# Kernel optimization log

Measured on AMD Instinct MI355X. Metric: run time of the kernel, lower is better.

## Reference

```python
import jax, jax.numpy as jnp
import numpy as np

VOCAB, EMB, HID, B, T = 32000, 1024, 1024, 16, 256

def setup_inputs() -> dict:
    key = jax.random.key(0)
    ks = jax.random.split(key, 9)
    s = 0.02
    return {
        "x": jax.random.randint(ks[0], (B, T), 0, VOCAB, dtype=jnp.int64),
        "hidden": jnp.zeros((2, B, HID), dtype=jnp.float32),
        "emb_W": jax.random.normal(ks[1], (VOCAB, EMB), dtype=jnp.float32) * s,  # tied with output proj
        "Wx0": jax.random.normal(ks[2], (EMB, HID), dtype=jnp.float32) * s,
        "Wh0": jax.random.normal(ks[3], (HID, HID), dtype=jnp.float32) * s,
        "b0": jnp.zeros((HID,), dtype=jnp.float32),
        "Wx1": jax.random.normal(ks[4], (HID, HID), dtype=jnp.float32) * s,
        "Wh1": jax.random.normal(ks[5], (HID, HID), dtype=jnp.float32) * s,
        "b1": jnp.zeros((HID,), dtype=jnp.float32),
        "out_b": jnp.zeros((VOCAB,), dtype=jnp.float32),
    }

def reference(x, hidden, emb_W, Wx0, Wh0, b0, Wx1, Wh1, b1, out_b):
    emb = emb_W[x]                      # (B, T, EMB)
    emb_t = jnp.swapaxes(emb, 0, 1)     # (T, B, EMB) time-major for scan

    def step(h, e):
        h0, h1 = h
        h0n = jnp.tanh(e @ Wx0 + h0 @ Wh0 + b0)      # layer 0 cell
        h1n = jnp.tanh(h0n @ Wx1 + h1 @ Wh1 + b1)    # layer 1 cell
        logits = h1n @ emb_W.T + out_b               # tied output projection
        return (h0n, h1n), logits

    (h0f, h1f), logits_t = jax.lax.scan(step, (hidden[0], hidden[1]), emb_t)
    logits = jnp.swapaxes(logits_t, 0, 1)            # (B, T, VOCAB)
    return logits, jnp.stack([h0f, h1f])             # final hidden (2, B, HID)
```

## Files before the change

kernel.cpp:

```cpp
#include <hip/hip_runtime.h>
#include <stdint.h>

#define VOCAB 32000
#define EMB   1024
#define HID   1024
#define BATCH 16
#define SEQ   256
#define MROWS (SEQ*BATCH)

typedef unsigned short u16;
typedef uint32_t u32;
typedef __bf16 bf16x8 __attribute__((ext_vector_type(8)));
typedef float  f32x4  __attribute__((ext_vector_type(4)));
typedef u32    u32x4  __attribute__((ext_vector_type(4)));

static __device__ __forceinline__ u16 f2bf(float f) {
  union { float f; uint32_t u; } v; v.f = f;
  return (u16)((v.u + 0x7FFFu + ((v.u >> 16) & 1u)) >> 16);
}

static __device__ __forceinline__ f32x4 MFMA(bf16x8 a, bf16x8 b, f32x4 c) {
  return __builtin_amdgcn_mfma_f32_16x16x32_bf16(a, b, c, 0, 0, 0);
}


static __device__ __forceinline__ void loadt8(const void* p, u32x4* r) {
  asm volatile(
    "global_load_dwordx4 %0, %8, off sc0 sc1\n\t"
    "global_load_dwordx4 %1, %8, off offset:16 sc0 sc1\n\t"
    "global_load_dwordx4 %2, %8, off offset:128 sc0 sc1\n\t"
    "global_load_dwordx4 %3, %8, off offset:144 sc0 sc1\n\t"
    "global_load_dwordx4 %4, %8, off offset:256 sc0 sc1\n\t"
    "global_load_dwordx4 %5, %8, off offset:272 sc0 sc1\n\t"
    "global_load_dwordx4 %6, %8, off offset:384 sc0 sc1\n\t"
    "global_load_dwordx4 %7, %8, off offset:400 sc0 sc1\n\t"
    "s_waitcnt vmcnt(0)"
    : "=&v"(r[0]), "=&v"(r[1]), "=&v"(r[2]), "=&v"(r[3]),
      "=&v"(r[4]), "=&v"(r[5]), "=&v"(r[6]), "=&v"(r[7])
    : "v"(p) : "memory");
}

static __device__ __forceinline__ void loadt16(const void* p, u32x4* r) {
  asm volatile(
    "global_load_dwordx4 %0, %16, off sc0 sc1\n\t"
    "global_load_dwordx4 %1, %16, off offset:16 sc0 sc1\n\t"
    "global_load_dwordx4 %2, %16, off offset:128 sc0 sc1\n\t"
    "global_load_dwordx4 %3, %16, off offset:144 sc0 sc1\n\t"
    "global_load_dwordx4 %4, %16, off offset:256 sc0 sc1\n\t"
    "global_load_dwordx4 %5, %16, off offset:272 sc0 sc1\n\t"
    "global_load_dwordx4 %6, %16, off offset:384 sc0 sc1\n\t"
    "global_load_dwordx4 %7, %16, off offset:400 sc0 sc1\n\t"
    "global_load_dwordx4 %8, %16, off offset:512 sc0 sc1\n\t"
    "global_load_dwordx4 %9, %16, off offset:528 sc0 sc1\n\t"
    "global_load_dwordx4 %10, %16, off offset:640 sc0 sc1\n\t"
    "global_load_dwordx4 %11, %16, off offset:656 sc0 sc1\n\t"
    "global_load_dwordx4 %12, %16, off offset:768 sc0 sc1\n\t"
    "global_load_dwordx4 %13, %16, off offset:784 sc0 sc1\n\t"
    "global_load_dwordx4 %14, %16, off offset:896 sc0 sc1\n\t"
    "global_load_dwordx4 %15, %16, off offset:912 sc0 sc1\n\t"
    "s_waitcnt vmcnt(0)"
    : "=&v"(r[0]), "=&v"(r[1]), "=&v"(r[2]), "=&v"(r[3]),
      "=&v"(r[4]), "=&v"(r[5]), "=&v"(r[6]), "=&v"(r[7]),
      "=&v"(r[8]), "=&v"(r[9]), "=&v"(r[10]), "=&v"(r[11]),
      "=&v"(r[12]), "=&v"(r[13]), "=&v"(r[14]), "=&v"(r[15])
    : "v"(p) : "memory");
}

static __device__ __forceinline__ void load22(const void* p0, const void* p1, u32x4* r) {
  asm volatile(
    "global_load_dwordx4 %0, %4, off sc0 sc1\n\t"
    "global_load_dwordx4 %1, %4, off offset:16 sc0 sc1\n\t"
    "global_load_dwordx4 %2, %5, off sc0 sc1\n\t"
    "global_load_dwordx4 %3, %5, off offset:16 sc0 sc1\n\t"
    "s_waitcnt vmcnt(0)"
    : "=&v"(r[0]), "=&v"(r[1]), "=&v"(r[2]), "=&v"(r[3])
    : "v"(p0), "v"(p1) : "memory");
}

static __device__ __forceinline__ void store_u32_coh(u32* p, u32 v) {
  asm volatile("global_store_dword %0, %1, off sc0 sc1"
               :: "v"(p), "v"(v) : "memory");
}
static __device__ __forceinline__ void store_u16_coh(u16* p, u16 v) {
  asm volatile("global_store_short %0, %1, off sc0 sc1"
               :: "v"(p), "v"((u32)v) : "memory");
}
static __device__ __forceinline__ void wait_vm0() {
  asm volatile("s_waitcnt vmcnt(0)" ::: "memory");
}

static __device__ __forceinline__ int flags_ready(const void* p, u32 pat) {
  u32x4 a, b, c, d;
  asm volatile(
    "global_load_dwordx4 %0, %4, off sc0 sc1\n\t"
    "global_load_dwordx4 %1, %4, off offset:16 sc0 sc1\n\t"
    "global_load_dwordx4 %2, %4, off offset:32 sc0 sc1\n\t"
    "global_load_dwordx4 %3, %4, off offset:48 sc0 sc1\n\t"
    "s_waitcnt vmcnt(0)"
    : "=&v"(a), "=&v"(b), "=&v"(c), "=&v"(d)
    : "v"(p) : "memory");
  u32 m = (a[0]^pat)|(a[1]^pat)|(a[2]^pat)|(a[3]^pat)
        | (b[0]^pat)|(b[1]^pat)|(b[2]^pat)|(b[3]^pat)
        | (c[0]^pat)|(c[1]^pat)|(c[2]^pat)|(c[3]^pat)
        | (d[0]^pat)|(d[1]^pat)|(d[2]^pat)|(d[3]^pat);
  return m == 0u;
}

static __device__ __forceinline__ bf16x8 packfrag(u32x4 e, u32x4 o) {
  u32x4 p;
  p[0] = (e[1] << 16) | (e[0] & 0xFFFFu);
  p[1] = (e[3] << 16) | (e[2] & 0xFFFFu);
  p[2] = (o[1] << 16) | (o[0] & 0xFFFFu);
  p[3] = (o[3] << 16) | (o[2] & 0xFFFFu);
  union { u32x4 u; bf16x8 b; } c; c.u = p; return c.b;
}


__global__ void cvt_hidden(const float* __restrict__ hidden,
                           u16* __restrict__ h0i, u16* __restrict__ h1i,
                           unsigned* __restrict__ flags) {
  int i = blockIdx.x * 256 + threadIdx.x;
  if (i < 16384) flags[i] = 0u;
  if (i < BATCH * HID)            h0i[i] = f2bf(hidden[i]);
  else if (i < 2 * BATCH * HID)   h1i[i - BATCH * HID] = f2bf(hidden[i]);
}

__global__ void transpose_cvt(const float* __restrict__ in, u16* __restrict__ out) {
  __shared__ float tile[32][33];
  int bx = blockIdx.x * 32;
  int by = blockIdx.y * 32;
  int tx = threadIdx.x, ty = threadIdx.y;
  #pragma unroll
  for (int i = 0; i < 32; i += 8)
    tile[ty + i][tx] = in[(size_t)(by + ty + i) * HID + bx + tx];
  __syncthreads();
  #pragma unroll
  for (int i = 0; i < 32; i += 8)
    out[(size_t)(bx + ty + i) * HID + by + tx] = f2bf(tile[tx][ty + i]);
}

__global__ void cvt_emb(const float4* __restrict__ in, ushort4* __restrict__ out, int n4) {
  int stride = gridDim.x * blockDim.x;
  for (int i = blockIdx.x * blockDim.x + threadIdx.x; i < n4; i += stride) {
    float4 v = in[i];
    ushort4 o; o.x = f2bf(v.x); o.y = f2bf(v.y); o.z = f2bf(v.z); o.w = f2bf(v.w);
    out[i] = o;
  }
}

__global__ void gather_emb(const int* __restrict__ x, const float* __restrict__ embW,
                           u16* __restrict__ E) {
  int r = blockIdx.x;
  int b = r & 15, t = r >> 4;
  int idx = x[b * SEQ + t];
  const float4* src = (const float4*)(embW + (size_t)idx * EMB);
  ushort4* dst = (ushort4*)(E + (size_t)r * EMB);
  float4 v = src[threadIdx.x];
  ushort4 o; o.x = f2bf(v.x); o.y = f2bf(v.y); o.z = f2bf(v.z); o.w = f2bf(v.w);
  dst[threadIdx.x] = o;
}

__global__ __launch_bounds__(256) void gemm_bt(
    const u16* __restrict__ A, const u16* __restrict__ B,
    const float* __restrict__ bias, float* __restrict__ C,
    int M, int N, int K)
{
  __shared__ __align__(16) char lds[32768];
  char* As = lds;
  char* Bs = lds + 16384;
  const int tid  = threadIdx.x;
  const int lane = tid & 63;
  const int wave = tid >> 6;
  const int wr = wave >> 1, wc = wave & 1;
  const int bm = blockIdx.y * 128;
  const int bn = blockIdx.x * 128;
  const int srow = tid >> 3;
  const int swc  = (tid & 7) ^ (srow & 7);

  f32x4 acc[4][4];
  #pragma unroll
  for (int i = 0; i < 4; ++i)
    #pragma unroll
    for (int j = 0; j < 4; ++j) acc[i][j] = (f32x4){0.f, 0.f, 0.f, 0.f};

  const u16* Ab = A + (size_t)(bm + srow) * K + swc * 8;
  const u16* Bb = B + (size_t)(bn + srow) * K + swc * 8;
  const size_t rstep = (size_t)32 * K;

  for (int k0 = 0; k0 < K; k0 += 64) {
    #pragma unroll
    for (int i = 0; i < 4; ++i) {
      __builtin_amdgcn_global_load_lds(
          (const __attribute__((address_space(1))) void*)(Ab + i * rstep + k0),
          (__attribute__((address_space(3))) void*)(As + i * 4096 + wave * 1024),
          16, 0, 0);
      __builtin_amdgcn_global_load_lds(
          (const __attribute__((address_space(1))) void*)(Bb + i * rstep + k0),
          (__attribute__((address_space(3))) void*)(Bs + i * 4096 + wave * 1024),
          16, 0, 0);
    }
    __syncthreads();
    #pragma unroll
    for (int ks = 0; ks < 2; ++ks) {
      bf16x8 af[4], bq[4];
      #pragma unroll
      for (int mi = 0; mi < 4; ++mi) {
        int row = wr * 64 + mi * 16 + (lane & 15);
        int c = (ks * 4 + (lane >> 4)) ^ (row & 7);
        af[mi] = *(const bf16x8*)(As + row * 128 + c * 16);
      }
      #pragma unroll
      for (int ni = 0; ni < 4; ++ni) {
        int row = wc * 64 + ni * 16 + (lane & 15);
        int c = (ks * 4 + (lane >> 4)) ^ (row & 7);
        bq[ni] = *(const bf16x8*)(Bs + row * 128 + c * 16);
      }
      #pragma unroll
      for (int mi = 0; mi < 4; ++mi)
        #pragma unroll
        for (int ni = 0; ni < 4; ++ni)
          acc[mi][ni] = MFMA(af[mi], bq[ni], acc[mi][ni]);
    }
    __syncthreads();
  }

  #pragma unroll
  for (int mi = 0; mi < 4; ++mi) {
    #pragma unroll
    for (int ni = 0; ni < 4; ++ni) {
      const int col = bn + wc * 64 + ni * 16 + (lane & 15);
      const float bv = bias[col];
      #pragma unroll
      for (int j = 0; j < 4; ++j) {
        const int row = bm + wr * 64 + mi * 16 + ((lane >> 4) << 2) + j;
        C[(size_t)row * N + col] = acc[mi][ni][j] + bv;
      }
    }
  }
}

#define NB0L 32
#define RL_NREC 64
#define LOG_TN 250
#define COMB_OFF 131072
#define LDS_TOTAL (COMB_OFF + 16384)

__global__ __launch_bounds__(512) void rec_logits(
    const u16* __restrict__ Wh0T, const u16* __restrict__ Wx1T, const u16* __restrict__ Wh1T,
    const float* __restrict__ X0, const float* __restrict__ b1,
    const u16* __restrict__ h0init, const u16* __restrict__ h1init,
    u32* H0u, u32* H1u,
    const u16* __restrict__ embB, const float* __restrict__ outb,
    float* out, char* flags)
{
  __shared__ __align__(16) char lds[LDS_TOTAL];
  const int tid  = threadIdx.x;
  const int lane = tid & 63;
  const int w    = tid >> 6;
  const int l15  = lane & 15;
  const int lk   = lane >> 4;
  const int blk  = blockIdx.x;
  f32x4* cmb = (f32x4*)(lds + COMB_OFF);
  float* hidOut = out + (size_t)BATCH * SEQ * VOCAB;

  if (blk >= RL_NREC) {
    const int lb = blk - RL_NREC;
    const int tm = lb / LOG_TN;
    const int tn = lb - tm * LOG_TN;
    const int bm = tm * 128, bn = tn * 128;
    if (tid == 0) {
      const u32 pat = (u32)(tm + 1) * 0x10001u;
      while (!flags_ready(flags + (size_t)tm * 128, pat)) __builtin_amdgcn_s_sleep(8);
    }
    __syncthreads();

    char* As = lds;
    char* Bs = lds + 16384;
    const int wr = w >> 2, wc = w & 3;
    const int srow = tid >> 3;
    const int sch  = (tid & 7) ^ (srow & 7);
    const u16* Bb  = embB + (size_t)(bn + srow) * EMB + sch * 8;
    const u32* Ab0 = H1u + (size_t)(bm + srow) * HID + sch * 8;
    const u32* Ab1 = H1u + (size_t)(bm + 64 + srow) * HID + sch * 8;
    char* Ad0 = As + srow * 128 + (tid & 7) * 16;
    char* Ad1 = As + (64 + srow) * 128 + (tid & 7) * 16;

    f32x4 acc[4][2];
    #pragma unroll
    for (int mi = 0; mi < 4; ++mi)
      #pragma unroll
      for (int ni = 0; ni < 2; ++ni) acc[mi][ni] = (f32x4){0.f, 0.f, 0.f, 0.f};

    for (int k0 = 0; k0 < EMB; k0 += 64) {
      #pragma unroll
      for (int i = 0; i < 2; ++i)
        __builtin_amdgcn_global_load_lds(
            (const __attribute__((address_space(1))) void*)(Bb + (size_t)i * 64 * EMB + k0),
            (__attribute__((address_space(3))) void*)(Bs + i * 8192 + w * 1024 + lane * 16),
            16, 0, 0);
      u32x4 ra[4];
      load22(Ab0 + k0, Ab1 + k0, ra);
      union { u32x4 u; bf16x8 b; } c0, c1;
      c0.b = packfrag(ra[0], ra[1]);
      c1.b = packfrag(ra[2], ra[3]);
      *(u32x4*)Ad0 = c0.u;
      *(u32x4*)Ad1 = c1.u;
      __syncthreads();
      #pragma unroll
      for (int ks = 0; ks < 2; ++ks) {
        bf16x8 af[4], bq[2];
        #pragma unroll
        for (int mi = 0; mi < 4; ++mi) {
          int row = wr * 64 + mi * 16 + l15;
          int c = (ks * 4 + lk) ^ (row & 7);
          af[mi] = *(const bf16x8*)(As + row * 128 + c * 16);
        }
        #pragma unroll
        for (int ni = 0; ni < 2; ++ni) {
          int row = wc * 32 + ni * 16 + l15;
          int c = (ks * 4 + lk) ^ (row & 7);
          bq[ni] = *(const bf16x8*)(Bs + row * 128 + c * 16);
        }
        #pragma unroll
        for (int mi = 0; mi < 4; ++mi)
          #pragma unroll
          for (int ni = 0; ni < 2; ++ni)
            acc[mi][ni] = MFMA(af[mi], bq[ni], acc[mi][ni]);
      }
      __syncthreads();
    }
    #pragma unroll
    for (int ni = 0; ni < 2; ++ni) {
      const int col = bn + wc * 32 + ni * 16 + l15;
      const float bv = outb[col];
      #pragma unroll
      for (int mi = 0; mi < 4; ++mi) {
        #pragma unroll
        for (int j = 0; j < 4; ++j) {
          const int row = bm + wr * 64 + mi * 16 + lk * 4 + j;
          out[(size_t)(row & 15) * ((size_t)SEQ * VOCAB)
              + (size_t)(row >> 4) * VOCAB + col] = acc[mi][ni][j] + bv;
        }
      }
    }
    return;
  }

  const bool is0 = (blk < NB0L);
  if (is0) {
    const u16* src = Wh0T + (size_t)(blk * 32) * HID;
    for (int it = 0; it < 8; ++it) {
      int g = it * 512 + tid;
      int brow = g & 31, f = g >> 5;
      *(bf16x8*)(lds + f * 512 + brow * 16) =
          *(const bf16x8*)(src + (size_t)brow * HID + f * 8);
    }
  } else {
    const u16* s0 = Wx1T + (size_t)((blk - NB0L) * 32) * HID;
    const u16* s1 = Wh1T + (size_t)((blk - NB0L) * 32) * HID;
    for (int it = 0; it < 8; ++it) {
      int g = it * 512 + tid;
      int brow = g & 31, f = g >> 5;
      int o = f * 512 + brow * 16;
      *(bf16x8*)(lds + o)         = *(const bf16x8*)(s0 + (size_t)brow * HID + f * 8);
      *(bf16x8*)(lds + 65536 + o) = *(const bf16x8*)(s1 + (size_t)brow * HID + f * 8);
    }
  }
  __syncthreads();

  if (is0) {
    const int col = blk * 32 + w * 16 + l15;
    const char* H0b = (const char*)H0u + (size_t)l15 * 4096 + (size_t)w * 512 + lk * 32;
    for (int s = 0; s < SEQ; ++s) {
      float xv[4];
      if (w < 2) {
        #pragma unroll
        for (int j = 0; j < 4; ++j)
          xv[j] = X0[(size_t)(s * BATCH + lk * 4 + j) * HID + col];
      }
      bf16x8 a[4];
      if (s == 0) {
        const char* p = (const char*)h0init + l15 * 2048 + w * 256 + lk * 16;
        #pragma unroll
        for (int m = 0; m < 4; ++m) a[m] = *(const bf16x8*)(p + m * 64);
      } else {
        u32x4 r[8];
        const void* hb = H0b + (size_t)(s - 1) * 65536;
        const u32 tagw = (u32)s << 16;
        for (;;) {
          loadt8(hb, r);
          u32 acc = 0;
          #pragma unroll
          for (int i = 0; i < 8; ++i)
            #pragma unroll
            for (int j = 0; j < 4; ++j) acc |= r[i][j] ^ tagw;
          if (__all((acc & 0xFFFF0000u) == 0u)) break;
        }
        #pragma unroll
        for (int m = 0; m < 4; ++m) a[m] = packfrag(r[2 * m], r[2 * m + 1]);
      }
      f32x4 acc0 = {0,0,0,0}, acc1 = {0,0,0,0};
      #pragma unroll
      for (int m = 0; m < 4; ++m) {
        const int f = (w * 4 + m) * 4 + lk;
        acc0 = MFMA(a[m], *(const bf16x8*)(lds + f * 512 + l15 * 16),        acc0);
        acc1 = MFMA(a[m], *(const bf16x8*)(lds + f * 512 + (16 + l15) * 16), acc1);
      }
      cmb[(w * 2 + 0) * 64 + lane] = acc0;
      cmb[(w * 2 + 1) * 64 + lane] = acc1;
      __syncthreads();
      if (w < 2) {
        f32x4 r = (cmb[(0 * 2 + w) * 64 + lane] + cmb[(1 * 2 + w) * 64 + lane])
                + (cmb[(2 * 2 + w) * 64 + lane] + cmb[(3 * 2 + w) * 64 + lane])
                + (cmb[(4 * 2 + w) * 64 + lane] + cmb[(5 * 2 + w) * 64 + lane])
                + (cmb[(6 * 2 + w) * 64 + lane] + cmb[(7 * 2 + w) * 64 + lane]);
        #pragma unroll
        for (int j = 0; j < 4; ++j) {
          const int b = lk * 4 + j;
          float v = tanhf(r[j] + xv[j]);
          u32 word = ((u32)(s + 1) << 16) | (u32)f2bf(v);
          store_u32_coh(H0u + (size_t)(s * BATCH + b) * HID + col, word);
          if (s == SEQ - 1) hidOut[(size_t)b * HID + col] = v;
        }
      }
      __syncthreads();
    }
  } else {
    const int lblk = blk - NB0L;
    const int m2 = w >> 2;
    const int q  = w & 3;
    const int col = lblk * 32 + w * 16 + l15;
    const float bv = (w < 2) ? b1[col] : 0.f;
    const char* wb = lds + m2 * 65536;
    const size_t lbase = (size_t)l15 * 4096 + (size_t)q * 1024 + lk * 32;
    for (int t = 0; t < SEQ; ++t) {
      bf16x8 a[8];
      if (m2 == 1 && t == 0) {
        const char* p = (const char*)h1init + l15 * 2048 + q * 512 + lk * 16;
        #pragma unroll
        for (int m = 0; m < 8; ++m) a[m] = *(const bf16x8*)(p + m * 64);
      } else {
        const void* hb = (m2 == 0)
            ? (const void*)((const char*)H0u + (size_t)t * 65536 + lbase)
            : (const void*)((const char*)H1u + (size_t)(t - 1) * 65536 + lbase);
        const u32 tagw = (u32)(m2 == 0 ? t + 1 : t) << 16;
        u32x4 r[16];
        for (;;) {
          loadt16(hb, r);
          u32 acc = 0;
          #pragma unroll
          for (int i = 0; i < 16; ++i)
            #pragma unroll
            for (int j = 0; j < 4; ++j) acc |= r[i][j] ^ tagw;
          if (__all((acc & 0xFFFF0000u) == 0u)) break;
        }
        #pragma unroll
        for (int m = 0; m < 8; ++m) a[m] = packfrag(r[2 * m], r[2 * m + 1]);
      }
      f32x4 acc0 = {0,0,0,0}, acc1 = {0,0,0,0};
      #pragma unroll
      for (int m = 0; m < 8; ++m) {
        const int f = (q * 8 + m) * 4 + lk;
        acc0 = MFMA(a[m], *(const bf16x8*)(wb + f * 512 + l15 * 16),        acc0);
        acc1 = MFMA(a[m], *(const bf16x8*)(wb + f * 512 + (16 + l15) * 16), acc1);
      }
      cmb[(w * 2 + 0) * 64 + lane] = acc0;
      cmb[(w * 2 + 1) * 64 + lane] = acc1;
      __syncthreads();
      if (w < 2) {
        f32x4 r = (cmb[(0 * 2 + w) * 64 + lane] + cmb[(1 * 2 + w) * 64 + lane])
                + (cmb[(2 * 2 + w) * 64 + lane] + cmb[(3 * 2 + w) * 64 + lane])
                + (cmb[(4 * 2 + w) * 64 + lane] + cmb[(5 * 2 + w) * 64 + lane])
                + (cmb[(6 * 2 + w) * 64 + lane] + cmb[(7 * 2 + w) * 64 + lane]);
        #pragma unroll
        for (int j = 0; j < 4; ++j) {
          const int b = lk * 4 + j;
          float v = tanhf(r[j] + bv);
          u32 word = ((u32)(t + 1) << 16) | (u32)f2bf(v);
          store_u32_coh(H1u + (size_t)(t * BATCH + b) * HID + col, word);
          if (t == SEQ - 1)
            hidOut[(size_t)(BATCH * HID) + (size_t)b * HID + col] = v;
        }
        if ((t & 7) == 7) wait_vm0();
      }
      __syncthreads();
      if (((t & 7) == 7) && tid == 0)
        store_u16_coh((u16*)(flags + (size_t)(t >> 3) * 128) + lblk, (u16)((t >> 3) + 1));
    }
  }
}

extern "C" void kernel_launch(void* const* d_in, const int* in_sizes, int n_in,
                              void* d_out, int out_size, void* d_ws, size_t ws_size,
                              hipStream_t stream) {
  const int*   x      = (const int*)  d_in[0];
  const float* hidden = (const float*)d_in[1];
  const float* embW   = (const float*)d_in[2];
  const float* Wx0    = (const float*)d_in[3];
  const float* Wh0    = (const float*)d_in[4];
  const float* b0     = (const float*)d_in[5];
  const float* Wx1    = (const float*)d_in[6];
  const float* Wh1    = (const float*)d_in[7];
  const float* b1     = (const float*)d_in[8];
  const float* outb   = (const float*)d_in[9];
  float* out = (float*)d_out;

  char* ws = (char*)d_ws;
  size_t off = 0;
  auto alloc = [&](size_t bytes) {
    char* p = ws + off; off += (bytes + 255) & ~(size_t)255; return p;
  };
  u16*   embB = (u16*)  alloc((size_t)VOCAB * EMB * 2);
  u16*   Wx0T = (u16*)  alloc((size_t)EMB * HID * 2);
  u16*   Wh0T = (u16*)  alloc((size_t)HID * HID * 2);
  u16*   Wx1T = (u16*)  alloc((size_t)HID * HID * 2);
  u16*   Wh1T = (u16*)  alloc((size_t)HID * HID * 2);
  u16*   E    = (u16*)  alloc((size_t)MROWS * EMB * 2);
  float* X0f  = (float*)alloc((size_t)MROWS * HID * 4);
  u32*   H0u  = (u32*)  alloc((size_t)MROWS * HID * 4);
  u32*   H1u  = (u32*)  alloc((size_t)MROWS * HID * 4);
  u16*   h0i  = (u16*)  alloc((size_t)BATCH * HID * 2);
  u16*   h1i  = (u16*)  alloc((size_t)BATCH * HID * 2);
  char*  flags = (char*)alloc(65536);
  if (off > ws_size) return;

  cvt_hidden<<<dim3(128), dim3(256), 0, stream>>>(hidden, h0i, h1i, (unsigned*)flags);

  dim3 tb(32, 8), tg(32, 32);
  transpose_cvt<<<tg, tb, 0, stream>>>(Wx0, Wx0T);
  transpose_cvt<<<tg, tb, 0, stream>>>(Wh0, Wh0T);
  transpose_cvt<<<tg, tb, 0, stream>>>(Wx1, Wx1T);
  transpose_cvt<<<tg, tb, 0, stream>>>(Wh1, Wh1T);

  cvt_emb<<<dim3(2048), dim3(256), 0, stream>>>(
      (const float4*)embW, (ushort4*)embB, (int)((size_t)VOCAB * EMB / 4));
  gather_emb<<<dim3(MROWS), dim3(256), 0, stream>>>(x, embW, E);

  gemm_bt<<<dim3(HID / 128, MROWS / 128), dim3(256), 0, stream>>>(
      E, Wx0T, b0, X0f, MROWS, HID, EMB);

  hipMemsetAsync(H0u, 0, (size_t)MROWS * HID * 4, stream);
  hipMemsetAsync(H1u, 0, (size_t)MROWS * HID * 4, stream);

  rec_logits<<<dim3(RL_NREC + 32 * LOG_TN), dim3(512), 0, stream>>>(
      Wh0T, Wx1T, Wh1T, X0f, b1, h0i, h1i, H0u, H1u, embB, outb, out, flags);
}
```

Baseline: 1.466 ms.

## Add repack blocks converting H1 to compact bf16 for direct LDS loads in logits

Adds 32 repack workgroups that wait for each 128-row chunk of the layer-1 hidden state, pack its u32-per-element storage into a contiguous bf16 buffer, and then set a per-chunk ready flag. The logits tiles wait on that single flag instead of scanning the full flag block. They then load A tiles straight into LDS with global_load_lds, with no register load, pack and LDS store per k-step. This halves A-operand traffic for each of the 250 column tiles and simplifies their inner loop. In exchange it adds an extra pass over H1, a second synchronization hop, and more launched workgroups.

```diff
diff --git a/kernel.cpp b/kernel.cpp
--- a/kernel.cpp
+++ b/kernel.cpp
@@ -66,17 +66,6 @@
     : "v"(p) : "memory");
 }
 
-static __device__ __forceinline__ void load22(const void* p0, const void* p1, u32x4* r) {
-  asm volatile(
-    "global_load_dwordx4 %0, %4, off sc0 sc1\n\t"
-    "global_load_dwordx4 %1, %4, off offset:16 sc0 sc1\n\t"
-    "global_load_dwordx4 %2, %5, off sc0 sc1\n\t"
-    "global_load_dwordx4 %3, %5, off offset:16 sc0 sc1\n\t"
-    "s_waitcnt vmcnt(0)"
-    : "=&v"(r[0]), "=&v"(r[1]), "=&v"(r[2]), "=&v"(r[3])
-    : "v"(p0), "v"(p1) : "memory");
-}
-
 static __device__ __forceinline__ void store_u32_coh(u32* p, u32 v) {
   asm volatile("global_store_dword %0, %1, off sc0 sc1"
                :: "v"(p), "v"(v) : "memory");
@@ -84,6 +73,11 @@
 static __device__ __forceinline__ void store_u16_coh(u16* p, u16 v) {
   asm volatile("global_store_short %0, %1, off sc0 sc1"
                :: "v"(p), "v"((u32)v) : "memory");
+}
+static __device__ __forceinline__ void store_u32x2_coh(void* p, u32 lo, u32 hi) {
+  union { u32 u[2]; uint2 v; } t; t.u[0] = lo; t.u[1] = hi;
+  asm volatile("global_store_dwordx2 %0, %1, off sc0 sc1"
+               :: "v"(p), "v"(t.v) : "memory");
 }
 static __device__ __forceinline__ void wait_vm0() {
   asm volatile("s_waitcnt vmcnt(0)" ::: "memory");
@@ -104,6 +98,13 @@
         | (c[0]^pat)|(c[1]^pat)|(c[2]^pat)|(c[3]^pat)
         | (d[0]^pat)|(d[1]^pat)|(d[2]^pat)|(d[3]^pat);
   return m == 0u;
+}
+
+static __device__ __forceinline__ int rdy_u32(const u32* p, u32 want) {
+  u32 v;
+  asm volatile("global_load_dword %0, %1, off sc0 sc1\n\ts_waitcnt vmcnt(0)"
+               : "=v"(v) : "v"(p) : "memory");
+  return v == want;
 }
 
 static __device__ __forceinline__ bf16x8 packfrag(u32x4 e, u32x4 o) {
@@ -241,6 +242,7 @@
 
 #define NB0L 32
 #define RL_NREC 64
+#define NREPACK 32
 #define LOG_TN 250
 #define COMB_OFF 131072
 #define LDS_TOTAL (COMB_OFF + 16384)
@@ -249,7 +251,7 @@
     const u16* __restrict__ Wh0T, const u16* __restrict__ Wx1T, const u16* __restrict__ Wh1T,
     const float* __restrict__ X0, const float* __restrict__ b1,
     const u16* __restrict__ h0init, const u16* __restrict__ h1init,
-    u32* H0u, u32* H1u,
+    u32* H0u, u32* H1u, u16* H1b,
     const u16* __restrict__ embB, const float* __restrict__ outb,
     float* out, char* flags)
 {
@@ -262,15 +264,15 @@
   const int blk  = blockIdx.x;
   f32x4* cmb = (f32x4*)(lds + COMB_OFF);
   float* hidOut = out + (size_t)BATCH * SEQ * VOCAB;
-
-  if (blk >= RL_NREC) {
-    const int lb = blk - RL_NREC;
+  u32* rf = (u32*)(flags + 32768);
+
+  if (blk >= RL_NREC + NREPACK) {
+    const int lb = blk - RL_NREC - NREPACK;
     const int tm = lb / LOG_TN;
     const int tn = lb - tm * LOG_TN;
     const int bm = tm * 128, bn = tn * 128;
     if (tid == 0) {
-      const u32 pat = (u32)(tm + 1) * 0x10001u;
-      while (!flags_ready(flags + (size_t)tm * 128, pat)) __builtin_amdgcn_s_sleep(8);
+      while (!rdy_u32(rf + (size_t)tm * 32, (u32)(tm + 1))) __builtin_amdgcn_s_sleep(8);
     }
     __syncthreads();
 
@@ -279,11 +281,8 @@
     const int wr = w >> 2, wc = w & 3;
     const int srow = tid >> 3;
     const int sch  = (tid & 7) ^ (srow & 7);
-    const u16* Bb  = embB + (size_t)(bn + srow) * EMB + sch * 8;
-    const u32* Ab0 = H1u + (size_t)(bm + srow) * HID + sch * 8;
-    const u32* Ab1 = H1u + (size_t)(bm + 64 + srow) * HID + sch * 8;
-    char* Ad0 = As + srow * 128 + (tid & 7) * 16;
-    char* Ad1 = As + (64 + srow) * 128 + (tid & 7) * 16;
+    const u16* Bb = embB + (size_t)(bn + srow) * EMB + sch * 8;
+    const u16* Ab = H1b  + (size_t)(bm + srow) * HID + sch * 8;
 
     f32x4 acc[4][2];
     #pragma unroll
@@ -293,18 +292,16 @@
 
     for (int k0 = 0; k0 < EMB; k0 += 64) {
       #pragma unroll
-      for (int i = 0; i < 2; ++i)
+      for (int i = 0; i < 2; ++i) {
         __builtin_amdgcn_global_load_lds(
             (const __attribute__((address_space(1))) void*)(Bb + (size_t)i * 64 * EMB + k0),
-            (__attribute__((address_space(3))) void*)(Bs + i * 8192 + w * 1024 + lane * 16),
+            (__attribute__((address_space(3))) void*)(Bs + i * 8192 + w * 1024),
             16, 0, 0);
-      u32x4 ra[4];
-      load22(Ab0 + k0, Ab1 + k0, ra);
-      union { u32x4 u; bf16x8 b; } c0, c1;
-      c0.b = packfrag(ra[0], ra[1]);
-      c1.b = packfrag(ra[2], ra[3]);
-      *(u32x4*)Ad0 = c0.u;
-      *(u32x4*)Ad1 = c1.u;
+        __builtin_amdgcn_global_load_lds(
+            (const __attribute__((address_space(1))) void*)(Ab + (size_t)i * 64 * HID + k0),
+            (__attribute__((address_space(3))) void*)(As + i * 8192 + w * 1024),
+            16, 0, 0);
+      }
       __syncthreads();
       #pragma unroll
       for (int ks = 0; ks < 2; ++ks) {
@@ -343,6 +340,29 @@
         }
       }
     }
+    return;
+  }
+
+  if (blk >= RL_NREC) {
+    const int g = blk - RL_NREC;
+    if (tid == 0) {
+      const u32 pat = (u32)(g + 1) * 0x10001u;
+      while (!flags_ready(flags + (size_t)g * 128, pat)) __builtin_amdgcn_s_sleep(2);
+    }
+    __syncthreads();
+    const u32* src = H1u + (size_t)g * 128 * 1024;
+    u16* dst = H1b + (size_t)g * 128 * 1024;
+    #pragma unroll 4
+    for (int i = 0; i < 64; ++i) {
+      int c = i * 512 + tid;
+      u32x4 v = *(const u32x4*)(src + (size_t)c * 4);
+      u32 lo = (v[0] & 0xFFFFu) | (v[1] << 16);
+      u32 hi = (v[2] & 0xFFFFu) | (v[3] << 16);
+      store_u32x2_coh(dst + (size_t)c * 4, lo, hi);
+    }
+    wait_vm0();
+    __syncthreads();
+    if (tid == 0) store_u32_coh(rf + (size_t)g * 32, (u32)(g + 1));
     return;
   }
 
@@ -519,6 +539,7 @@
   float* X0f  = (float*)alloc((size_t)MROWS * HID * 4);
   u32*   H0u  = (u32*)  alloc((size_t)MROWS * HID * 4);
   u32*   H1u  = (u32*)  alloc((size_t)MROWS * HID * 4);
+  u16*   H1b  = (u16*)  alloc((size_t)MROWS * HID * 2);
   u16*   h0i  = (u16*)  alloc((size_t)BATCH * HID * 2);
   u16*   h1i  = (u16*)  alloc((size_t)BATCH * HID * 2);
   char*  flags = (char*)alloc(65536);
@@ -542,6 +563,6 @@
   hipMemsetAsync(H0u, 0, (size_t)MROWS * HID * 4, stream);
   hipMemsetAsync(H1u, 0, (size_t)MROWS * HID * 4, stream);
 
-  rec_logits<<<dim3(RL_NREC + 32 * LOG_TN), dim3(512), 0, stream>>>(
-      Wh0T, Wx1T, Wh1T, X0f, b1, h0i, h1i, H0u, H1u, embB, outb, out, flags);
-}
+  rec_logits<<<dim3(RL_NREC + NREPACK + 32 * LOG_TN), dim3(512), 0, stream>>>(
+      Wh0T, Wx1T, Wh1T, X0f, b1, h0i, h1i, H0u, H1u, H1b, embB, outb, out, flags);
+}
```

New measurement: 1.440 ms (median of 2 runs). About the same (-1.8%).
